# Kernel tuning notes

Measured on AMD Instinct MI355X. Metric: run time of the kernel, lower is better.

## Reference

```python
import jax, jax.numpy as jnp
import numpy as np

N, F, A = 50000, 128, 128

def setup_inputs() -> dict:
    key = jax.random.key(0)
    ks = jax.random.split(key, 20)
    r = lambda i, shape: jax.random.normal(ks[i], shape, dtype=jnp.float32)
    w = lambda i, shape: jax.random.normal(ks[i], shape, dtype=jnp.float32) * 0.05
    return {
        "feat": r(0, (N, F)),
        "mu": r(1, (N, F, 3)),
        "T0": r(2, (N,)),
        "T1": r(3, (N, 3)),
        "T2": r(4, (N, 3, 3)),
        "T3": r(5, (N, 3, 3, 3)),
        # denseq: Dense(F,F,swish) -> Dense(F,F). Weights stored [in,out].
        "Wq1": w(6, (F, F)), "bq1": jnp.zeros((F,), jnp.float32),
        "Wq2": w(7, (F, F)), "bq2": jnp.zeros((F,), jnp.float32),
        "WT1": w(8, (F, F)),  # dense_T1, no bias
        "WT2": w(9, (F, F)),  # dense_T2, no bias
        "WT3": w(10, (F, F)), # dense_T3, no bias
        # dense_s: Dense(F,F,swish) -> Dense(F,A)
        "Ws1": w(11, (F, F)), "bs1": jnp.zeros((F,), jnp.float32),
        "Ws2": w(12, (F, A)), "bs2": jnp.zeros((A,), jnp.float32),
        "Wv": w(13, (F, A)),  # dense_v, no bias
    }

def reference(feat, mu, T0, T1, T2, T3,
              Wq1, bq1, Wq2, bq2, WT1, WT2, WT3,
              Ws1, bs1, Ws2, bs2, Wv):
    silu = jax.nn.silu  # swish
    # M0 = denseq(feat): [N, F]
    M0 = silu(feat @ Wq1 + bq1) @ Wq2 + bq2
    # M1/M2/M3: linear over feature dim of mu [N, F, 3]
    M1 = jnp.einsum('nfc,fg->ngc', mu, WT1)
    M2 = jnp.einsum('nfc,fg->ngc', mu, WT2)
    M3 = jnp.einsum('nfc,fg->ngc', mu, WT3)
    # scalar channel
    ms = jnp.sum(M1 * T1[:, None, :], axis=-1) + T0[:, None] * M0          # T1, T0 terms
    ms = ms + jnp.einsum('nfi,nfj,nij->nf', M2, M2, T2)                    # quadrupole . T2
    ms = ms + jnp.einsum('nfi,nfj,nfk,nijk->nf', M3, M3, M3, T3)           # octupole . T3
    # vector channel [N, F, 3]
    mv = T1[:, None, :] * M0[..., None]
    mv = mv + jnp.einsum('nij,nfj->nfi', T2, M1)
    mv = mv + jnp.einsum('nijk,nfj,nfk->nfi', T3, M2, M2)
    # output projections
    mv_out = jnp.einsum('nfc,fa->nac', mv, Wv)                             # [N, A, 3]
    ms_out = silu(ms @ Ws1 + bs1) @ Ws2 + bs2                              # [N, A]
    return ms_out, mv_out
```

## Files before the change

kernel.cpp:

```cpp
#include <hip/hip_runtime.h>
#include <cstdint>

#define N_NODES 50000
#define TILE 32
#define NBLK ((N_NODES + TILE - 1) / TILE)

typedef __bf16 bf16x8 __attribute__((ext_vector_type(8)));
typedef unsigned short ushort8_t __attribute__((ext_vector_type(8)));
typedef float f32x4 __attribute__((ext_vector_type(4)));

__device__ __forceinline__ unsigned short f2bf(float x) {
  union { float f; uint32_t u; } v; v.f = x;
  uint32_t r = v.u + 0x7FFFu + ((v.u >> 16) & 1u);
  return (unsigned short)(r >> 16);
}

__device__ __forceinline__ float fast_silu(float x) {
  return x / (1.0f + __expf(-x));
}

__global__ __launch_bounds__(256) void prep_weights(
    const float* __restrict__ Wq1, const float* __restrict__ Wq2,
    const float* __restrict__ WT1, const float* __restrict__ WT2,
    const float* __restrict__ WT3, const float* __restrict__ Ws1,
    const float* __restrict__ Ws2, const float* __restrict__ Wv,
    unsigned short* __restrict__ ws) {
  int tid = blockIdx.x * 256 + threadIdx.x;
  int w = tid >> 11;
  int rest = tid & 2047;
  int c = rest >> 8;
  int kt = (rest >> 6) & 3;
  int lane = rest & 63;
  int g = (lane & 15) + 16 * c;
  int k0 = kt * 32 + (lane >> 4) * 8;
  const float* srcs[8] = {Wq1, Wq2, WT1, WT2, WT3, Ws1, Ws2, Wv};
  const float* src = srcs[w];
  union { unsigned short u[8]; uint4 v; } o;
#pragma unroll
  for (int j = 0; j < 8; ++j) o.u[j] = f2bf(src[(k0 + j) * 128 + g]);
  *(uint4*)(ws + (size_t)w * 16384 + (size_t)rest * 8) = o.v;
}

__device__ __forceinline__ bf16x8 ldB(const unsigned short* __restrict__ wg,
                                      int c, int kt, int lane) {
  return __builtin_bit_cast(
      bf16x8, *(const ushort8_t*)(wg + (((c * 4 + kt) * 64 + lane)) * 8));
}

__device__ __forceinline__ void gemm16g(const unsigned short* __restrict__ sA,
                                        const unsigned short* __restrict__ wg,
                                        int lane, int cb, f32x4 acc[2][2]) {
  const int m = lane & 15, q = lane >> 4;
  const f32x4 vzero = {0.f, 0.f, 0.f, 0.f};
#pragma unroll
  for (int rt = 0; rt < 2; ++rt)
#pragma unroll
    for (int cc = 0; cc < 2; ++cc) acc[rt][cc] = vzero;
#pragma unroll
  for (int kt = 0; kt < 4; ++kt) {
    const int k0 = q * 8 + kt * 32;
    bf16x8 a0 = __builtin_bit_cast(bf16x8, *(const ushort8_t*)(sA + m * 136 + k0));
    bf16x8 a1 = __builtin_bit_cast(bf16x8, *(const ushort8_t*)(sA + (m + 16) * 136 + k0));
#pragma unroll
    for (int cc = 0; cc < 2; ++cc) {
      bf16x8 b = ldB(wg, cb + cc, kt, lane);
      acc[0][cc] = __builtin_amdgcn_mfma_f32_16x16x32_bf16(a0, b, acc[0][cc], 0, 0, 0);
      acc[1][cc] = __builtin_amdgcn_mfma_f32_16x16x32_bf16(a1, b, acc[1][cc], 0, 0, 0);
    }
  }
}

__device__ __forceinline__ void gemm3g(const unsigned short* __restrict__ s0,
                                       const unsigned short* __restrict__ s1,
                                       const unsigned short* __restrict__ s2,
                                       const unsigned short* __restrict__ wg,
                                       int lane, int cb,
                                       f32x4 A1[2][2], f32x4 A2[2][2],
                                       f32x4 A3[2][2]) {
  const int m = lane & 15, q = lane >> 4;
  const f32x4 vzero = {0.f, 0.f, 0.f, 0.f};
#pragma unroll
  for (int rt = 0; rt < 2; ++rt)
#pragma unroll
    for (int cc = 0; cc < 2; ++cc) {
      A1[rt][cc] = vzero; A2[rt][cc] = vzero; A3[rt][cc] = vzero;
    }
#pragma unroll
  for (int kt = 0; kt < 4; ++kt) {
    const int k0 = q * 8 + kt * 32;
    bf16x8 a00 = __builtin_bit_cast(bf16x8, *(const ushort8_t*)(s0 + m * 136 + k0));
    bf16x8 a01 = __builtin_bit_cast(bf16x8, *(const ushort8_t*)(s0 + (m + 16) * 136 + k0));
    bf16x8 a10 = __builtin_bit_cast(bf16x8, *(const ushort8_t*)(s1 + m * 136 + k0));
    bf16x8 a11 = __builtin_bit_cast(bf16x8, *(const ushort8_t*)(s1 + (m + 16) * 136 + k0));
    bf16x8 a20 = __builtin_bit_cast(bf16x8, *(const ushort8_t*)(s2 + m * 136 + k0));
    bf16x8 a21 = __builtin_bit_cast(bf16x8, *(const ushort8_t*)(s2 + (m + 16) * 136 + k0));
#pragma unroll
    for (int cc = 0; cc < 2; ++cc) {
      bf16x8 b = ldB(wg, cb + cc, kt, lane);
      A1[0][cc] = __builtin_amdgcn_mfma_f32_16x16x32_bf16(a00, b, A1[0][cc], 0, 0, 0);
      A1[1][cc] = __builtin_amdgcn_mfma_f32_16x16x32_bf16(a01, b, A1[1][cc], 0, 0, 0);
      A2[0][cc] = __builtin_amdgcn_mfma_f32_16x16x32_bf16(a10, b, A2[0][cc], 0, 0, 0);
      A2[1][cc] = __builtin_amdgcn_mfma_f32_16x16x32_bf16(a11, b, A2[1][cc], 0, 0, 0);
      A3[0][cc] = __builtin_amdgcn_mfma_f32_16x16x32_bf16(a20, b, A3[0][cc], 0, 0, 0);
      A3[1][cc] = __builtin_amdgcn_mfma_f32_16x16x32_bf16(a21, b, A3[1][cc], 0, 0, 0);
    }
  }
}

__global__ __launch_bounds__(256, 2) void multipole_main(
    const float* __restrict__ feat, const float* __restrict__ mu,
    const float* __restrict__ T0g, const float* __restrict__ T1g,
    const float* __restrict__ T2g, const float* __restrict__ T3g,
    const float* __restrict__ bq1, const float* __restrict__ bq2,
    const float* __restrict__ bs1, const float* __restrict__ bs2,
    const unsigned short* __restrict__ ws, float* __restrict__ out) {
  __shared__ unsigned short sXmain[TILE * 136];
  __shared__ unsigned short sXmu[3][TILE * 136];
  __shared__ float sT[TILE][47];

  const int t = threadIdx.x;
  const int lane = t & 63, wv = t >> 6;
  const int m = lane & 15, q = lane >> 4;
  const int cb = wv * 2;
  const int nodeBase = blockIdx.x * TILE;

  {
    int node = t >> 3, f0 = (t & 7) * 16;
    int gn = nodeBase + node;
    union { unsigned short u[16]; uint4 v[2]; } buf;
    if (gn < N_NODES) {
      const float4* p = (const float4*)(feat + (size_t)gn * 128 + f0);
      float xs[16];
#pragma unroll
      for (int i = 0; i < 4; ++i) *(float4*)(xs + 4 * i) = p[i];
#pragma unroll
      for (int i = 0; i < 16; ++i) buf.u[i] = f2bf(xs[i]);
    } else {
#pragma unroll
      for (int i = 0; i < 16; ++i) buf.u[i] = 0;
    }
    uint4* dst = (uint4*)&sXmain[node * 136 + f0];
    dst[0] = buf.v[0]; dst[1] = buf.v[1];
  }

  {
    int node = t >> 3, f0 = (t & 7) * 16;
    int gn = nodeBase + node;
    union { unsigned short u[16]; uint4 v[2]; } b3[3];
    if (gn < N_NODES) {
      const float4* p = (const float4*)(mu + ((size_t)gn * 128 + f0) * 3);
      float xs[48];
#pragma unroll
      for (int i = 0; i < 12; ++i) *(float4*)(xs + 4 * i) = p[i];
#pragma unroll
      for (int i = 0; i < 16; ++i) {
        b3[0].u[i] = f2bf(xs[i * 3 + 0]);
        b3[1].u[i] = f2bf(xs[i * 3 + 1]);
        b3[2].u[i] = f2bf(xs[i * 3 + 2]);
      }
    } else {
#pragma unroll
      for (int ch = 0; ch < 3; ++ch)
#pragma unroll
        for (int i = 0; i < 16; ++i) b3[ch].u[i] = 0;
    }
#pragma unroll
    for (int ch = 0; ch < 3; ++ch) {
      uint4* dst = (uint4*)&sXmu[ch][node * 136 + f0];
      dst[0] = b3[ch].v[0]; dst[1] = b3[ch].v[1];
    }
  }

  if (t < TILE) {
    int n = nodeBase + t;
    bool val = n < N_NODES;
    float t0 = val ? T0g[n] : 0.f;
    float t1[3], t2[9], t3[27];
#pragma unroll
    for (int i = 0; i < 3; ++i) t1[i] = val ? T1g[n * 3 + i] : 0.f;
#pragma unroll
    for (int i = 0; i < 9; ++i) t2[i] = val ? T2g[n * 9 + i] : 0.f;
#pragma unroll
    for (int i = 0; i < 27; ++i) t3[i] = val ? T3g[n * 27 + i] : 0.f;
    float* Tr = sT[t];
    Tr[0] = t0;
    Tr[1] = t1[0]; Tr[2] = t1[1]; Tr[3] = t1[2];
#pragma unroll
    for (int i = 0; i < 9; ++i) Tr[4 + i] = t2[i];
    Tr[13] = t2[0]; Tr[14] = t2[1] + t2[3]; Tr[15] = t2[2] + t2[6];
    Tr[16] = t2[4]; Tr[17] = t2[5] + t2[7]; Tr[18] = t2[8];
    Tr[19] = t3[0];
    Tr[20] = t3[1] + t3[3] + t3[9];
    Tr[21] = t3[2] + t3[6] + t3[18];
    Tr[22] = t3[4] + t3[10] + t3[12];
    Tr[23] = t3[5] + t3[7] + t3[11] + t3[15] + t3[19] + t3[21];
    Tr[24] = t3[8] + t3[20] + t3[24];
    Tr[25] = t3[13];
    Tr[26] = t3[14] + t3[16] + t3[22];
    Tr[27] = t3[17] + t3[23] + t3[25];
    Tr[28] = t3[26];
#pragma unroll
    for (int i = 0; i < 3; ++i) {
      const float* b = t3 + 9 * i;
      float* d = Tr + 29 + 6 * i;
      d[0] = b[0]; d[1] = b[1] + b[3]; d[2] = b[2] + b[6];
      d[3] = b[4]; d[4] = b[5] + b[7]; d[5] = b[8];
    }
  }
  __syncthreads();

  f32x4 A1[2][2], A2[2][2], A3[2][2];
  float msv[2][2][4];
  float mvv[3][2][2][4];

  gemm16g(sXmain, ws, lane, cb, A1);
  float b0 = bq1[cb * 16 + m], b1 = bq1[cb * 16 + 16 + m];
  __syncthreads();
#pragma unroll
  for (int rt = 0; rt < 2; ++rt)
#pragma unroll
    for (int ri = 0; ri < 4; ++ri) {
      int lrow = rt * 16 + q * 4 + ri;
#pragma unroll
      for (int cc = 0; cc < 2; ++cc) {
        float h = fast_silu(A1[rt][cc][ri] + (cc ? b1 : b0));
        sXmain[lrow * 136 + (cb + cc) * 16 + m] = f2bf(h);
      }
    }
  __syncthreads();

  gemm16g(sXmain, ws + 1 * 16384, lane, cb, A1);
  {
    float bb0 = bq2[cb * 16 + m], bb1 = bq2[cb * 16 + 16 + m];
#pragma unroll
    for (int rt = 0; rt < 2; ++rt)
#pragma unroll
      for (int ri = 0; ri < 4; ++ri) {
        const float* Tr = sT[rt * 16 + q * 4 + ri];
        float t0 = Tr[0], ta = Tr[1], tb = Tr[2], tc = Tr[3];
#pragma unroll
        for (int cc = 0; cc < 2; ++cc) {
          float m0 = A1[rt][cc][ri] + (cc ? bb1 : bb0);
          msv[rt][cc][ri] = t0 * m0;
          mvv[0][rt][cc][ri] = ta * m0;
          mvv[1][rt][cc][ri] = tb * m0;
          mvv[2][rt][cc][ri] = tc * m0;
        }
      }
  }

#pragma unroll
  for (int ch = 0; ch < 3; ++ch) {
    gemm16g(sXmu[ch], ws + 2 * 16384, lane, cb, A1);
#pragma unroll
    for (int rt = 0; rt < 2; ++rt)
#pragma unroll
      for (int ri = 0; ri < 4; ++ri) {
        const float* Tr = sT[rt * 16 + q * 4 + ri];
        float t1c = Tr[1 + ch];
        float u0 = Tr[4 + 0 + ch], u1 = Tr[4 + 3 + ch], u2 = Tr[4 + 6 + ch];
#pragma unroll
        for (int cc = 0; cc < 2; ++cc) {
          float v = A1[rt][cc][ri];
          msv[rt][cc][ri] += t1c * v;
          mvv[0][rt][cc][ri] += u0 * v;
          mvv[1][rt][cc][ri] += u1 * v;
          mvv[2][rt][cc][ri] += u2 * v;
        }
      }
  }

  gemm16g(sXmu[0], ws + 4 * 16384, lane, cb, A1);
  gemm16g(sXmu[1], ws + 4 * 16384, lane, cb, A2);
  gemm16g(sXmu[2], ws + 4 * 16384, lane, cb, A3);
#pragma unroll
  for (int rt = 0; rt < 2; ++rt)
#pragma unroll
    for (int ri = 0; ri < 4; ++ri) {
      const float* Cp = sT[rt * 16 + q * 4 + ri] + 19;
      float c0 = Cp[0], c1 = Cp[1], c2 = Cp[2], c3 = Cp[3], c4 = Cp[4];
      float c5 = Cp[5], c6 = Cp[6], c7 = Cp[7], c8 = Cp[8], c9 = Cp[9];
#pragma unroll
      for (int cc = 0; cc < 2; ++cc) {
        float u0 = A1[rt][cc][ri], u1 = A2[rt][cc][ri], u2 = A3[rt][cc][ri];
        float Q0 = u0 * u0, Q1 = u0 * u1, Q2 = u0 * u2;
        float Q3 = u1 * u1, Q4 = u1 * u2, Q5 = u2 * u2;
        msv[rt][cc][ri] += c0 * (Q0 * u0) + c1 * (Q0 * u1) + c2 * (Q0 * u2) +
                           c3 * (Q1 * u1) + c4 * (Q1 * u2) + c5 * (Q2 * u2) +
                           c6 * (Q3 * u1) + c7 * (Q3 * u2) + c8 * (Q4 * u2) +
                           c9 * (Q5 * u2);
      }
    }

  gemm16g(sXmu[0], ws + 3 * 16384, lane, cb, A1);
  gemm16g(sXmu[1], ws + 3 * 16384, lane, cb, A2);
  gemm16g(sXmu[2], ws + 3 * 16384, lane, cb, A3);
#pragma unroll
  for (int rt = 0; rt < 2; ++rt)
#pragma unroll
    for (int ri = 0; ri < 4; ++ri) {
      const float* Tr = sT[rt * 16 + q * 4 + ri];
      const float* q2 = Tr + 13;
      const float* d3 = Tr + 29;
      float q20 = q2[0], q21 = q2[1], q22 = q2[2], q23 = q2[3], q24 = q2[4], q25 = q2[5];
#pragma unroll
      for (int cc = 0; cc < 2; ++cc) {
        float v0 = A1[rt][cc][ri], v1 = A2[rt][cc][ri], v2 = A3[rt][cc][ri];
        float P0 = v0 * v0, P1 = v0 * v1, P2 = v0 * v2;
        float P3 = v1 * v1, P4 = v1 * v2, P5 = v2 * v2;
        msv[rt][cc][ri] += q20 * P0 + q21 * P1 + q22 * P2 + q23 * P3 + q24 * P4 + q25 * P5;
        mvv[0][rt][cc][ri] += d3[0] * P0 + d3[1] * P1 + d3[2] * P2 + d3[3] * P3 + d3[4] * P4 + d3[5] * P5;
        mvv[1][rt][cc][ri] += d3[6] * P0 + d3[7] * P1 + d3[8] * P2 + d3[9] * P3 + d3[10] * P4 + d3[11] * P5;
        mvv[2][rt][cc][ri] += d3[12] * P0 + d3[13] * P1 + d3[14] * P2 + d3[15] * P3 + d3[16] * P4 + d3[17] * P5;
      }
    }
  __syncthreads();

#pragma unroll
  for (int rt = 0; rt < 2; ++rt)
#pragma unroll
    for (int ri = 0; ri < 4; ++ri) {
      int lrow = rt * 16 + q * 4 + ri;
#pragma unroll
      for (int cc = 0; cc < 2; ++cc) {
        int col = (cb + cc) * 16 + m;
        sXmain[lrow * 136 + col] = f2bf(msv[rt][cc][ri]);
        sXmu[0][lrow * 136 + col] = f2bf(mvv[0][rt][cc][ri]);
        sXmu[1][lrow * 136 + col] = f2bf(mvv[1][rt][cc][ri]);
        sXmu[2][lrow * 136 + col] = f2bf(mvv[2][rt][cc][ri]);
      }
    }
  __syncthreads();

  gemm16g(sXmain, ws + 5 * 16384, lane, cb, A1);
  {
    float s0 = bs1[cb * 16 + m], s1 = bs1[cb * 16 + 16 + m];
    __syncthreads();
#pragma unroll
    for (int rt = 0; rt < 2; ++rt)
#pragma unroll
      for (int ri = 0; ri < 4; ++ri) {
        int lrow = rt * 16 + q * 4 + ri;
#pragma unroll
        for (int cc = 0; cc < 2; ++cc) {
          float g = fast_silu(A1[rt][cc][ri] + (cc ? s1 : s0));
          sXmain[lrow * 136 + (cb + cc) * 16 + m] = f2bf(g);
        }
      }
  }
  __syncthreads();

  gemm16g(sXmain, ws + 6 * 16384, lane, cb, A1);
  {
    float s0 = bs2[cb * 16 + m], s1 = bs2[cb * 16 + 16 + m];
#pragma unroll
    for (int rt = 0; rt < 2; ++rt)
#pragma unroll
      for (int ri = 0; ri < 4; ++ri) {
        int grow = nodeBase + rt * 16 + q * 4 + ri;
        if (grow < N_NODES) {
#pragma unroll
          for (int cc = 0; cc < 2; ++cc) {
            int col = (cb + cc) * 16 + m;
            out[(size_t)grow * 128 + col] = A1[rt][cc][ri] + (cc ? s1 : s0);
          }
        }
      }
  }

  float* out2 = out + (size_t)N_NODES * 128;
  gemm3g(sXmu[0], sXmu[1], sXmu[2], ws + 7 * 16384, lane, cb, A1, A2, A3);
#pragma unroll
  for (int rt = 0; rt < 2; ++rt)
#pragma unroll
    for (int ri = 0; ri < 4; ++ri) {
      int grow = nodeBase + rt * 16 + q * 4 + ri;
      if (grow < N_NODES) {
#pragma unroll
        for (int cc = 0; cc < 2; ++cc) {
          int col = (cb + cc) * 16 + m;
          float* p = out2 + ((size_t)grow * 128 + col) * 3;
          p[0] = A1[rt][cc][ri];
          p[1] = A2[rt][cc][ri];
          p[2] = A3[rt][cc][ri];
        }
      }
    }
}

extern "C" void kernel_launch(void* const* d_in, const int* in_sizes, int n_in,
                              void* d_out, int out_size, void* d_ws, size_t ws_size,
                              hipStream_t stream) {
  const float* feat = (const float*)d_in[0];
  const float* mu   = (const float*)d_in[1];
  const float* T0   = (const float*)d_in[2];
  const float* T1   = (const float*)d_in[3];
  const float* T2   = (const float*)d_in[4];
  const float* T3   = (const float*)d_in[5];
  const float* Wq1  = (const float*)d_in[6];
  const float* bq1  = (const float*)d_in[7];
  const float* Wq2  = (const float*)d_in[8];
  const float* bq2  = (const float*)d_in[9];
  const float* WT1  = (const float*)d_in[10];
  const float* WT2  = (const float*)d_in[11];
  const float* WT3  = (const float*)d_in[12];
  const float* Ws1  = (const float*)d_in[13];
  const float* bs1  = (const float*)d_in[14];
  const float* Ws2  = (const float*)d_in[15];
  const float* bs2  = (const float*)d_in[16];
  const float* Wv   = (const float*)d_in[17];
  unsigned short* ws = (unsigned short*)d_ws;
  float* out = (float*)d_out;

  prep_weights<<<64, 256, 0, stream>>>(Wq1, Wq2, WT1, WT2, WT3, Ws1, Ws2, Wv, ws);
  multipole_main<<<NBLK, 256, 0, stream>>>(feat, mu, T0, T1, T2, T3,
                                           bq1, bq2, bs1, bs2, ws, out);
}
```

Measured before the change: 307.6 us.

## Stage weights through LDS and batch mu-channel GEMMs into three-way MFMA passes

Each bf16 weight matrix is now copied into a 32 KB shared buffer before its GEMM instead of being read per-lane from global memory. The three per-channel GEMMs for WT1 and WT2 are merged into the three-input gemm3L, so each B fragment is read once per three channels. The mu load is deferred until after the feature MLP, and f2bf uses the native bf16 conversion. This adds many extra __syncthreads and 32 KB of LDS per block, which may lower occupancy and serialize weight staging against compute.

```diff
diff --git a/kernel.cpp b/kernel.cpp
--- a/kernel.cpp
+++ b/kernel.cpp
@@ -10,9 +10,7 @@
 typedef float f32x4 __attribute__((ext_vector_type(4)));
 
 __device__ __forceinline__ unsigned short f2bf(float x) {
-  union { float f; uint32_t u; } v; v.f = x;
-  uint32_t r = v.u + 0x7FFFu + ((v.u >> 16) & 1u);
-  return (unsigned short)(r >> 16);
+  return __builtin_bit_cast(unsigned short, (__bf16)x);
 }
 
 __device__ __forceinline__ float fast_silu(float x) {
@@ -41,15 +39,9 @@
   *(uint4*)(ws + (size_t)w * 16384 + (size_t)rest * 8) = o.v;
 }
 
-__device__ __forceinline__ bf16x8 ldB(const unsigned short* __restrict__ wg,
-                                      int c, int kt, int lane) {
-  return __builtin_bit_cast(
-      bf16x8, *(const ushort8_t*)(wg + (((c * 4 + kt) * 64 + lane)) * 8));
-}
-
-__device__ __forceinline__ void gemm16g(const unsigned short* __restrict__ sA,
-                                        const unsigned short* __restrict__ wg,
-                                        int lane, int cb, f32x4 acc[2][2]) {
+__device__ __forceinline__ void gemm16(const unsigned short* sA,
+                                       const unsigned short* sWp,
+                                       int lane, int cb, f32x4 acc[2][2]) {
   const int m = lane & 15, q = lane >> 4;
   const f32x4 vzero = {0.f, 0.f, 0.f, 0.f};
 #pragma unroll
@@ -63,17 +55,18 @@
     bf16x8 a1 = __builtin_bit_cast(bf16x8, *(const ushort8_t*)(sA + (m + 16) * 136 + k0));
 #pragma unroll
     for (int cc = 0; cc < 2; ++cc) {
-      bf16x8 b = ldB(wg, cb + cc, kt, lane);
+      bf16x8 b = __builtin_bit_cast(
+          bf16x8, *(const ushort8_t*)(sWp + (((cb + cc) * 4 + kt) * 64 + lane) * 8));
       acc[0][cc] = __builtin_amdgcn_mfma_f32_16x16x32_bf16(a0, b, acc[0][cc], 0, 0, 0);
       acc[1][cc] = __builtin_amdgcn_mfma_f32_16x16x32_bf16(a1, b, acc[1][cc], 0, 0, 0);
     }
   }
 }
 
-__device__ __forceinline__ void gemm3g(const unsigned short* __restrict__ s0,
-                                       const unsigned short* __restrict__ s1,
-                                       const unsigned short* __restrict__ s2,
-                                       const unsigned short* __restrict__ wg,
+__device__ __forceinline__ void gemm3L(const unsigned short* s0,
+                                       const unsigned short* s1,
+                                       const unsigned short* s2,
+                                       const unsigned short* sWp,
                                        int lane, int cb,
                                        f32x4 A1[2][2], f32x4 A2[2][2],
                                        f32x4 A3[2][2]) {
@@ -96,7 +89,8 @@
     bf16x8 a21 = __builtin_bit_cast(bf16x8, *(const ushort8_t*)(s2 + (m + 16) * 136 + k0));
 #pragma unroll
     for (int cc = 0; cc < 2; ++cc) {
-      bf16x8 b = ldB(wg, cb + cc, kt, lane);
+      bf16x8 b = __builtin_bit_cast(
+          bf16x8, *(const ushort8_t*)(sWp + (((cb + cc) * 4 + kt) * 64 + lane) * 8));
       A1[0][cc] = __builtin_amdgcn_mfma_f32_16x16x32_bf16(a00, b, A1[0][cc], 0, 0, 0);
       A1[1][cc] = __builtin_amdgcn_mfma_f32_16x16x32_bf16(a01, b, A1[1][cc], 0, 0, 0);
       A2[0][cc] = __builtin_amdgcn_mfma_f32_16x16x32_bf16(a10, b, A2[0][cc], 0, 0, 0);
@@ -114,9 +108,10 @@
     const float* __restrict__ bq1, const float* __restrict__ bq2,
     const float* __restrict__ bs1, const float* __restrict__ bs2,
     const unsigned short* __restrict__ ws, float* __restrict__ out) {
+  __shared__ unsigned short sW[16384];
   __shared__ unsigned short sXmain[TILE * 136];
   __shared__ unsigned short sXmu[3][TILE * 136];
-  __shared__ float sT[TILE][47];
+  __shared__ float sT[TILE][49];
 
   const int t = threadIdx.x;
   const int lane = t & 63, wv = t >> 6;
@@ -124,52 +119,12 @@
   const int cb = wv * 2;
   const int nodeBase = blockIdx.x * TILE;
 
-  {
-    int node = t >> 3, f0 = (t & 7) * 16;
-    int gn = nodeBase + node;
-    union { unsigned short u[16]; uint4 v[2]; } buf;
-    if (gn < N_NODES) {
-      const float4* p = (const float4*)(feat + (size_t)gn * 128 + f0);
-      float xs[16];
-#pragma unroll
-      for (int i = 0; i < 4; ++i) *(float4*)(xs + 4 * i) = p[i];
-#pragma unroll
-      for (int i = 0; i < 16; ++i) buf.u[i] = f2bf(xs[i]);
-    } else {
-#pragma unroll
-      for (int i = 0; i < 16; ++i) buf.u[i] = 0;
-    }
-    uint4* dst = (uint4*)&sXmain[node * 136 + f0];
-    dst[0] = buf.v[0]; dst[1] = buf.v[1];
-  }
-
-  {
-    int node = t >> 3, f0 = (t & 7) * 16;
-    int gn = nodeBase + node;
-    union { unsigned short u[16]; uint4 v[2]; } b3[3];
-    if (gn < N_NODES) {
-      const float4* p = (const float4*)(mu + ((size_t)gn * 128 + f0) * 3);
-      float xs[48];
-#pragma unroll
-      for (int i = 0; i < 12; ++i) *(float4*)(xs + 4 * i) = p[i];
-#pragma unroll
-      for (int i = 0; i < 16; ++i) {
-        b3[0].u[i] = f2bf(xs[i * 3 + 0]);
-        b3[1].u[i] = f2bf(xs[i * 3 + 1]);
-        b3[2].u[i] = f2bf(xs[i * 3 + 2]);
-      }
-    } else {
-#pragma unroll
-      for (int ch = 0; ch < 3; ++ch)
-#pragma unroll
-        for (int i = 0; i < 16; ++i) b3[ch].u[i] = 0;
-    }
-#pragma unroll
-    for (int ch = 0; ch < 3; ++ch) {
-      uint4* dst = (uint4*)&sXmu[ch][node * 136 + f0];
-      dst[0] = b3[ch].v[0]; dst[1] = b3[ch].v[1];
-    }
-  }
+  auto stage_w = [&](int slot) {
+    const uint4* src = (const uint4*)(ws + (size_t)slot * 16384);
+    uint4* dst = (uint4*)sW;
+#pragma unroll
+    for (int i = 0; i < 8; ++i) dst[t + i * 256] = src[t + i * 256];
+  };
 
   if (t < TILE) {
     int n = nodeBase + t;
@@ -207,13 +162,33 @@
       d[3] = b[4]; d[4] = b[5] + b[7]; d[5] = b[8];
     }
   }
+
+  {
+    int node = t >> 3, f0 = (t & 7) * 16;
+    int gn = nodeBase + node;
+    union { unsigned short u[16]; uint4 v[2]; } buf;
+    if (gn < N_NODES) {
+      const float4* p = (const float4*)(feat + (size_t)gn * 128 + f0);
+      float xs[16];
+#pragma unroll
+      for (int i = 0; i < 4; ++i) *(float4*)(xs + 4 * i) = p[i];
+#pragma unroll
+      for (int i = 0; i < 16; ++i) buf.u[i] = f2bf(xs[i]);
+    } else {
+#pragma unroll
+      for (int i = 0; i < 16; ++i) buf.u[i] = 0;
+    }
+    uint4* dst = (uint4*)&sXmain[node * 136 + f0];
+    dst[0] = buf.v[0]; dst[1] = buf.v[1];
+  }
+  stage_w(0);
   __syncthreads();
 
   f32x4 A1[2][2], A2[2][2], A3[2][2];
   float msv[2][2][4];
   float mvv[3][2][2][4];
 
-  gemm16g(sXmain, ws, lane, cb, A1);
+  gemm16(sXmain, sW, lane, cb, A1);
   float b0 = bq1[cb * 16 + m], b1 = bq1[cb * 16 + 16 + m];
   __syncthreads();
 #pragma unroll
@@ -227,9 +202,10 @@
         sXmain[lrow * 136 + (cb + cc) * 16 + m] = f2bf(h);
       }
     }
-  __syncthreads();
-
-  gemm16g(sXmain, ws + 1 * 16384, lane, cb, A1);
+  stage_w(1);
+  __syncthreads();
+
+  gemm16(sXmain, sW, lane, cb, A1);
   {
     float bb0 = bq2[cb * 16 + m], bb1 = bq2[cb * 16 + 16 + m];
 #pragma unroll
@@ -248,31 +224,58 @@
         }
       }
   }
-
-#pragma unroll
-  for (int ch = 0; ch < 3; ++ch) {
-    gemm16g(sXmu[ch], ws + 2 * 16384, lane, cb, A1);
-#pragma unroll
-    for (int rt = 0; rt < 2; ++rt)
-#pragma unroll
-      for (int ri = 0; ri < 4; ++ri) {
-        const float* Tr = sT[rt * 16 + q * 4 + ri];
-        float t1c = Tr[1 + ch];
-        float u0 = Tr[4 + 0 + ch], u1 = Tr[4 + 3 + ch], u2 = Tr[4 + 6 + ch];
-#pragma unroll
-        for (int cc = 0; cc < 2; ++cc) {
-          float v = A1[rt][cc][ri];
-          msv[rt][cc][ri] += t1c * v;
-          mvv[0][rt][cc][ri] += u0 * v;
-          mvv[1][rt][cc][ri] += u1 * v;
-          mvv[2][rt][cc][ri] += u2 * v;
-        }
-      }
-  }
-
-  gemm16g(sXmu[0], ws + 4 * 16384, lane, cb, A1);
-  gemm16g(sXmu[1], ws + 4 * 16384, lane, cb, A2);
-  gemm16g(sXmu[2], ws + 4 * 16384, lane, cb, A3);
+  __syncthreads();
+
+  {
+    int node = t >> 3, f0 = (t & 7) * 16;
+    int gn = nodeBase + node;
+    union { unsigned short u[16]; uint4 v[2]; } b3[3];
+    if (gn < N_NODES) {
+      const float4* p = (const float4*)(mu + ((size_t)gn * 128 + f0) * 3);
+      float xs[48];
+#pragma unroll
+      for (int i = 0; i < 12; ++i) *(float4*)(xs + 4 * i) = p[i];
+#pragma unroll
+      for (int i = 0; i < 16; ++i) {
+        b3[0].u[i] = f2bf(xs[i * 3 + 0]);
+        b3[1].u[i] = f2bf(xs[i * 3 + 1]);
+        b3[2].u[i] = f2bf(xs[i * 3 + 2]);
+      }
+    } else {
+#pragma unroll
+      for (int ch = 0; ch < 3; ++ch)
+#pragma unroll
+        for (int i = 0; i < 16; ++i) b3[ch].u[i] = 0;
+    }
+#pragma unroll
+    for (int ch = 0; ch < 3; ++ch) {
+      uint4* dst = (uint4*)&sXmu[ch][node * 136 + f0];
+      dst[0] = b3[ch].v[0]; dst[1] = b3[ch].v[1];
+    }
+  }
+  stage_w(2);
+  __syncthreads();
+
+  gemm3L(sXmu[0], sXmu[1], sXmu[2], sW, lane, cb, A1, A2, A3);
+#pragma unroll
+  for (int rt = 0; rt < 2; ++rt)
+#pragma unroll
+    for (int ri = 0; ri < 4; ++ri) {
+      const float* Tr = sT[rt * 16 + q * 4 + ri];
+#pragma unroll
+      for (int cc = 0; cc < 2; ++cc) {
+        float v0 = A1[rt][cc][ri], v1 = A2[rt][cc][ri], v2 = A3[rt][cc][ri];
+        msv[rt][cc][ri] += Tr[1] * v0 + Tr[2] * v1 + Tr[3] * v2;
+        mvv[0][rt][cc][ri] += Tr[4] * v0 + Tr[5] * v1 + Tr[6] * v2;
+        mvv[1][rt][cc][ri] += Tr[7] * v0 + Tr[8] * v1 + Tr[9] * v2;
+        mvv[2][rt][cc][ri] += Tr[10] * v0 + Tr[11] * v1 + Tr[12] * v2;
+      }
+    }
+  __syncthreads();
+  stage_w(4);
+  __syncthreads();
+
+  gemm3L(sXmu[0], sXmu[1], sXmu[2], sW, lane, cb, A1, A2, A3);
 #pragma unroll
   for (int rt = 0; rt < 2; ++rt)
 #pragma unroll
@@ -291,10 +294,11 @@
                            c9 * (Q5 * u2);
       }
     }
-
-  gemm16g(sXmu[0], ws + 3 * 16384, lane, cb, A1);
-  gemm16g(sXmu[1], ws + 3 * 16384, lane, cb, A2);
-  gemm16g(sXmu[2], ws + 3 * 16384, lane, cb, A3);
+  __syncthreads();
+  stage_w(3);
+  __syncthreads();
+
+  gemm3L(sXmu[0], sXmu[1], sXmu[2], sW, lane, cb, A1, A2, A3);
 #pragma unroll
   for (int rt = 0; rt < 2; ++rt)
 #pragma unroll
@@ -330,9 +334,10 @@
         sXmu[2][lrow * 136 + col] = f2bf(mvv[2][rt][cc][ri]);
       }
     }
-  __syncthreads();
-
-  gemm16g(sXmain, ws + 5 * 16384, lane, cb, A1);
+  stage_w(5);
+  __syncthreads();
+
+  gemm16(sXmain, sW, lane, cb, A1);
   {
     float s0 = bs1[cb * 16 + m], s1 = bs1[cb * 16 + 16 + m];
     __syncthreads();
@@ -348,9 +353,10 @@
         }
       }
   }
-  __syncthreads();
-
-  gemm16g(sXmain, ws + 6 * 16384, lane, cb, A1);
+  stage_w(6);
+  __syncthreads();
+
+  gemm16(sXmain, sW, lane, cb, A1);
   {
     float s0 = bs2[cb * 16 + m], s1 = bs2[cb * 16 + 16 + m];
 #pragma unroll
@@ -367,9 +373,12 @@
         }
       }
   }
+  __syncthreads();
+  stage_w(7);
+  __syncthreads();
 
   float* out2 = out + (size_t)N_NODES * 128;
-  gemm3g(sXmu[0], sXmu[1], sXmu[2], ws + 7 * 16384, lane, cb, A1, A2, A3);
+  gemm3L(sXmu[0], sXmu[1], sXmu[2], sW, lane, cb, A1, A2, A3);
 #pragma unroll
   for (int rt = 0; rt < 2; ++rt)
 #pragma unroll
```

After: 272.1 us. 11.5% less time.
